# Kernel tuning notes

Hardware: AMD Instinct MI355X
Metric: run time of the kernel (lower is better)

## Reference

```python
import jax, jax.numpy as jnp
import numpy as np

B, T, V, U = 128, 256, 256, 2048


def setup_inputs() -> dict:
    key = jax.random.key(0)
    k_x, k_wx, k_wh, k_wd = jax.random.split(key, 4)
    x = jax.random.randint(k_x, (B, T), 0, V)
    # glorot-ish scaling so tanh doesn't saturate
    Wx = jax.random.normal(k_wx, (V, U), jnp.float32) * (1.0 / np.sqrt(V))
    Wh = jax.random.normal(k_wh, (U, U), jnp.float32) * (1.0 / np.sqrt(U))
    b = jnp.zeros((U,), jnp.float32)
    Wd = jax.random.normal(k_wd, (U, V), jnp.float32) * (1.0 / np.sqrt(U))
    bd = jnp.zeros((V,), jnp.float32)
    h0 = jnp.zeros((B, U), jnp.float32)
    return {"x": x, "Wx": Wx, "Wh": Wh, "b": b, "Wd": Wd, "bd": bd, "h0": h0}


def reference(x, Wx, Wh, b, Wd, bd, h0):
    # one_hot(x, V) @ Wx  ==  Wx[x]  (row gather; avoids materializing one-hot)
    x_proj = Wx[x] + b  # [B, T, U]
    x_proj_t = jnp.swapaxes(x_proj, 0, 1)  # [T, B, U] for scan

    def step(h, xt):
        # SimpleRNN cell: h_t = tanh(x_t Wx + h_{t-1} Wh + b)
        h_new = jnp.tanh(xt + h @ Wh)
        return h_new, h_new

    _, hs = jax.lax.scan(step, h0, x_proj_t)  # hs: [T, B, U]
    hs = jnp.swapaxes(hs, 0, 1)  # [B, T, U]
    logits = jnp.einsum('btu,uv->btv', hs, Wd) + bd  # [B, T, V]
    return logits
```

## Files before the change

### kernel.cpp

```cpp
#include <hip/hip_runtime.h>
#include <hip/hip_bf16.h>

#define B_ 128
#define T_ 256
#define V_ 256
#define U_ 2048

typedef __bf16 bf16x8 __attribute__((ext_vector_type(8)));
typedef float f32x4 __attribute__((ext_vector_type(4)));
typedef unsigned u32x4 __attribute__((ext_vector_type(4)));

union B8u { uint4 u; bf16x8 v; };

static __device__ inline bf16x8 u2b(uint4 u) { B8u t; t.u = u; return t.v; }
static __device__ inline bf16x8 ldg8(const unsigned short* p) {
    B8u t; t.u = *reinterpret_cast<const uint4*>(p); return t.v;
}
static __device__ inline bf16x8 lds8(const char* smem, unsigned off) {
    B8u t; t.u = *reinterpret_cast<const uint4*>(smem + off); return t.v;
}
static __device__ inline unsigned short f2b(float f) {
    __hip_bfloat16 h = __float2bfloat16(f);
    unsigned short r; __builtin_memcpy(&r, &h, 2); return r;
}
static __device__ inline uint4 ldg16_c(const unsigned short* p) {
    uint4 r;
    asm volatile("global_load_dwordx4 %0, %1, off"
                 : "=&v"(r) : "v"(p) : "memory");
    return r;
}
static __device__ inline void stg16_sc(unsigned short* p, u32x4 v) {
    asm volatile("global_store_dwordx4 %0, %1, off sc0 sc1"
                 :: "v"(p), "v"(v) : "memory");
}
static __device__ inline void stg4_sc_u32(unsigned* p, unsigned v) {
    asm volatile("global_store_dword %0, %1, off sc0 sc1"
                 :: "v"(p), "v"(v) : "memory");
}
static __device__ inline uint4 ldg16_sc_wait(const unsigned* p) {
    uint4 r;
    asm volatile("global_load_dwordx4 %0, %1, off sc0 sc1\n\ts_waitcnt vmcnt(0)"
                 : "=&v"(r) : "v"(p) : "memory");
    return r;
}
static __device__ inline float tanh_fast(float x) {
    float e = __expf(2.0f * x);
    return 1.0f - 2.0f * __builtin_amdgcn_rcpf(e + 1.0f);
}


__global__ void transpose_bf16(const float* __restrict__ in,
                               unsigned short* __restrict__ outp, int R, int C) {
    __shared__ float tile[32][33];
    int tc = blockIdx.x * 32, tr = blockIdx.y * 32;
    int lx = threadIdx.x & 31, ly = threadIdx.x >> 5;
#pragma unroll
    for (int i = 0; i < 32; i += 8)
        tile[ly + i][lx] = in[(size_t)(tr + ly + i) * C + tc + lx];
    __syncthreads();
#pragma unroll
    for (int i = 0; i < 32; i += 8)
        outp[(size_t)(tc + ly + i) * R + tr + lx] = f2b(tile[lx][ly + i]);
}

__global__ void prep_misc(const float* __restrict__ h0, unsigned short* __restrict__ hb,
                          const int* __restrict__ x, int* __restrict__ xT) {
    int i = blockIdx.x * 256 + threadIdx.x;
    hb[i] = f2b(h0[i]);
    if (i < B_ * T_) {
        int b = i >> 8, t = i & 255;
        xT[t * B_ + b] = x[i];
    }
}

__global__ __launch_bounds__(256, 1) void rnn_arc9(
        const int* __restrict__ xT, const float* __restrict__ Wx,
        const float* __restrict__ bias, const unsigned short* __restrict__ WhT,
        unsigned short* __restrict__ hs, unsigned* __restrict__ flags) {
    extern __shared__ char smem[];
    float* red = (float*)(smem + 32 * 2048 * 2);

    const int bid = blockIdx.x;
    const int g = bid >> 6, p = bid & 63;
    const int b0 = g * 32, c0 = p * 32;
    const int tid = threadIdx.x;
    const int w = tid >> 6, lane = tid & 63;
    const int lr = lane & 15, lh = lane >> 4;

    for (int i = tid; i < 32 * 256; i += 256) {
        int c = i >> 8, k8 = i & 255;
        uint4 v = *reinterpret_cast<const uint4*>(WhT + (size_t)(c0 + c) * U_ + k8 * 8);
        unsigned off = (unsigned)(c * 4096 + k8 * 16) ^ ((unsigned)(c & 7) << 4);
        *reinterpret_cast<uint4*>(smem + off) = v;
    }
    __syncthreads();

    const int kbase = w * 512;
    const unsigned lin0 = (unsigned)(lr * 4096) + (unsigned)((kbase + lh * 8) * 2);
    const unsigned lin1 = lin0 + 16 * 4096;
    const unsigned swz = (unsigned)(lr & 7) << 4;

    const bool epi = tid < 128;
    const int erow = tid >> 2;
    const int ec8 = (tid & 3) * 8;
    const int ucol = c0 + ec8;
    f32x4 bias4a = {0, 0, 0, 0}, bias4b = {0, 0, 0, 0};
    if (epi) {
        bias4a = *reinterpret_cast<const f32x4*>(bias + ucol);
        bias4b = *reinterpret_cast<const f32x4*>(bias + ucol + 4);
    }

    unsigned* myflag = flags + (unsigned)(g * 256 + p * 4 + w);
    const unsigned* pollp = flags + (unsigned)(g * 256 + lane * 4);

    f32x4 xpa = {0, 0, 0, 0}, xpb = {0, 0, 0, 0};
    if (epi) {
        int tok = xT[0 * B_ + b0 + erow];
        const float* wr = Wx + (size_t)tok * U_ + ucol;
        xpa = *reinterpret_cast<const f32x4*>(wr) + bias4a;
        xpb = *reinterpret_cast<const f32x4*>(wr + 4) + bias4b;
    }

    for (int t = 0; t < T_; ++t) {
        const unsigned short* hp = hs + (size_t)t * (B_ * U_);
        unsigned short* hc = hs + (size_t)(t + 1) * (B_ * U_);

        const unsigned short* pa0 = hp + (size_t)(b0 + lr) * U_ + kbase + lh * 8;
        const unsigned short* pa1 = pa0 + 16 * U_;
        uint4 areg0[16], areg1[16];
#pragma unroll
        for (int ks = 0; ks < 16; ++ks) {
            areg0[ks] = ldg16_c(pa0 + ks * 32);
            areg1[ks] = ldg16_c(pa1 + ks * 32);
        }
        asm volatile("s_waitcnt vmcnt(0)" ::: "memory");
        __builtin_amdgcn_sched_barrier(0);

        f32x4 acc00 = {0.f, 0.f, 0.f, 0.f}, acc01 = {0.f, 0.f, 0.f, 0.f};
        f32x4 acc10 = {0.f, 0.f, 0.f, 0.f}, acc11 = {0.f, 0.f, 0.f, 0.f};
#pragma unroll
        for (int ks = 0; ks < 16; ++ks) {
            bf16x8 a0 = u2b(areg0[ks]);
            bf16x8 a1 = u2b(areg1[ks]);
            bf16x8 bb0 = lds8(smem, (lin0 + (unsigned)ks * 64u) ^ swz);
            bf16x8 bb1 = lds8(smem, (lin1 + (unsigned)ks * 64u) ^ swz);
            acc00 = __builtin_amdgcn_mfma_f32_16x16x32_bf16(a0, bb0, acc00, 0, 0, 0);
            acc01 = __builtin_amdgcn_mfma_f32_16x16x32_bf16(a0, bb1, acc01, 0, 0, 0);
            acc10 = __builtin_amdgcn_mfma_f32_16x16x32_bf16(a1, bb0, acc10, 0, 0, 0);
            acc11 = __builtin_amdgcn_mfma_f32_16x16x32_bf16(a1, bb1, acc11, 0, 0, 0);
        }

        float* redw = red + w * 1152;
#pragma unroll
        for (int r = 0; r < 4; ++r) {
            redw[(lh * 4 + r) * 36 + lr] = acc00[r];
            redw[(lh * 4 + r) * 36 + 16 + lr] = acc01[r];
            redw[(16 + lh * 4 + r) * 36 + lr] = acc10[r];
            redw[(16 + lh * 4 + r) * 36 + 16 + lr] = acc11[r];
        }
        __syncthreads();

        if (epi) {
            const int o = erow * 36 + ec8;
            f32x4 za = *reinterpret_cast<f32x4*>(red + 0 * 1152 + o);
            f32x4 zb = *reinterpret_cast<f32x4*>(red + 0 * 1152 + o + 4);
            za += *reinterpret_cast<f32x4*>(red + 1 * 1152 + o);
            zb += *reinterpret_cast<f32x4*>(red + 1 * 1152 + o + 4);
            za += *reinterpret_cast<f32x4*>(red + 2 * 1152 + o);
            zb += *reinterpret_cast<f32x4*>(red + 2 * 1152 + o + 4);
            za += *reinterpret_cast<f32x4*>(red + 3 * 1152 + o);
            zb += *reinterpret_cast<f32x4*>(red + 3 * 1152 + o + 4);
            za += xpa;
            zb += xpb;
            u32x4 pk;
            pk.x = (unsigned)f2b(tanh_fast(za[0])) | ((unsigned)f2b(tanh_fast(za[1])) << 16);
            pk.y = (unsigned)f2b(tanh_fast(za[2])) | ((unsigned)f2b(tanh_fast(za[3])) << 16);
            pk.z = (unsigned)f2b(tanh_fast(zb[0])) | ((unsigned)f2b(tanh_fast(zb[1])) << 16);
            pk.w = (unsigned)f2b(tanh_fast(zb[2])) | ((unsigned)f2b(tanh_fast(zb[3])) << 16);
            stg16_sc(hc + (size_t)(b0 + erow) * U_ + ucol, pk);
        }

        asm volatile("s_waitcnt vmcnt(0)" ::: "memory");
        if (lane == 0) stg4_sc_u32(myflag, (unsigned)(t + 1));

        if (epi && t + 1 < T_) {
            int tok = xT[(t + 1) * B_ + b0 + erow];
            const float* wr = Wx + (size_t)tok * U_ + ucol;
            xpa = *reinterpret_cast<const f32x4*>(wr) + bias4a;
            xpb = *reinterpret_cast<const f32x4*>(wr + 4) + bias4b;
        }

        if (t + 1 < T_) {
            if (w == 0) {
                for (;;) {
                    uint4 f = ldg16_sc_wait(pollp);
                    unsigned m01 = f.x < f.y ? f.x : f.y;
                    unsigned m23 = f.z < f.w ? f.z : f.w;
                    unsigned m = m01 < m23 ? m01 : m23;
                    if (__all(m > (unsigned)t)) break;
                    __builtin_amdgcn_s_sleep(1);
                }
            }
            __syncthreads();
        }
    }
}

__global__ __launch_bounds__(256, 2) void decode_gemm2(
        const unsigned short* __restrict__ hsD, const unsigned short* __restrict__ WdT,
        const float* __restrict__ bdv, float* __restrict__ out) {
    const int tid = threadIdx.x;
    const int w = tid >> 6, lane = tid & 63;
    const int lr = lane & 15, lh = lane >> 4;
    const int r0 = blockIdx.x * 32;
    const int v0 = w * 64;

    const unsigned short* pa0 = hsD + (size_t)(r0 + lr) * U_ + lh * 8;
    const unsigned short* pa1 = pa0 + (size_t)16 * U_;
    const unsigned short* pb0 = WdT + (size_t)(v0 + lr) * U_ + lh * 8;

    f32x4 acc0[4], acc1[4];
#pragma unroll
    for (int n = 0; n < 4; ++n) {
        acc0[n] = (f32x4){0.f, 0.f, 0.f, 0.f};
        acc1[n] = (f32x4){0.f, 0.f, 0.f, 0.f};
    }

#pragma unroll 4
    for (int ks = 0; ks < 64; ++ks) {
        bf16x8 a0 = ldg8(pa0 + ks * 32);
        bf16x8 a1 = ldg8(pa1 + ks * 32);
#pragma unroll
        for (int n = 0; n < 4; ++n) {
            bf16x8 bb = ldg8(pb0 + (size_t)n * 16 * U_ + ks * 32);
            acc0[n] = __builtin_amdgcn_mfma_f32_16x16x32_bf16(a0, bb, acc0[n], 0, 0, 0);
            acc1[n] = __builtin_amdgcn_mfma_f32_16x16x32_bf16(a1, bb, acc1[n], 0, 0, 0);
        }
    }

#pragma unroll
    for (int n = 0; n < 4; ++n) {
        float bd_ = bdv[v0 + n * 16 + lr];
#pragma unroll
        for (int r = 0; r < 4; ++r) {
            int m0 = r0 + lh * 4 + r;
            int m1 = m0 + 16;
            out[((size_t)(m0 & 127) * T_ + (m0 >> 7)) * V_ + v0 + n * 16 + lr] =
                acc0[n][r] + bd_;
            out[((size_t)(m1 & 127) * T_ + (m1 >> 7)) * V_ + v0 + n * 16 + lr] =
                acc1[n][r] + bd_;
        }
    }
}

extern "C" void kernel_launch(void* const* d_in, const int* in_sizes, int n_in,
                              void* d_out, int out_size, void* d_ws, size_t ws_size,
                              hipStream_t stream) {
    const int* x = (const int*)d_in[0];
    const float* Wx = (const float*)d_in[1];
    const float* Wh = (const float*)d_in[2];
    const float* b = (const float*)d_in[3];
    const float* Wd = (const float*)d_in[4];
    const float* bd = (const float*)d_in[5];
    const float* h0 = (const float*)d_in[6];
    float* out = (float*)d_out;

    char* ws = (char*)d_ws;

    const size_t OFF_WhT = 0;
    const size_t OFF_WdT = 8388608;
    const size_t OFF_xT = 9437184;
    const size_t OFF_FLG = 9568256;
    const size_t OFF_HS = 9572352;

    unsigned short* WhT = (unsigned short*)(ws + OFF_WhT);
    unsigned short* WdT = (unsigned short*)(ws + OFF_WdT);
    int* xT = (int*)(ws + OFF_xT);
    unsigned* flags = (unsigned*)(ws + OFF_FLG);
    unsigned short* hs = (unsigned short*)(ws + OFF_HS);

    hipMemsetAsync(flags, 0, 4096, stream);
    transpose_bf16<<<dim3(64, 64), 256, 0, stream>>>(Wh, WhT, 2048, 2048);
    transpose_bf16<<<dim3(8, 64), 256, 0, stream>>>(Wd, WdT, 2048, 256);
    prep_misc<<<1024, 256, 0, stream>>>(h0, hs, x, xT);

    const int smem_bytes = 32 * 2048 * 2 + 4 * 1152 * 4;
    hipFuncSetAttribute((const void*)rnn_arc9, hipFuncAttributeMaxDynamicSharedMemorySize,
                        smem_bytes);
    void* args[] = {(void*)&xT, (void*)&Wx, (void*)&b, (void*)&WhT, (void*)&hs,
                    (void*)&flags};
    hipLaunchCooperativeKernel((const void*)rnn_arc9, dim3(256), dim3(256), args,
                               (unsigned)smem_bytes, stream);

    const unsigned short* hsD = hs + (size_t)B_ * U_;
    decode_gemm2<<<1024, 256, 0, stream>>>(hsD, WdT, bd, out);
}
```

Measured before the change: 1.800 ms.

## Fuse output projection into persistent RNN kernel using idle blocks per step

The decoder GEMM (hs @ Wd + bd) moves into the cooperative recurrent kernel. At each step, the first 16 column blocks of each batch group reuse the h_{t} tiles already loaded in registers to compute logits for step t-1 against a register-resident slice of WdT, with a one-step-delayed LDS reduction and store. This removes the separate decode kernel and its re-read of the full hidden-state history, but adds MFMA work, register pressure and LDS to every block's serial critical path. A fallback to the old two-kernel path is kept for when occupancy is insufficient.

```diff
diff --git a/kernel.cpp b/kernel.cpp
--- a/kernel.cpp
+++ b/kernel.cpp
@@ -73,12 +73,15 @@
     }
 }
 
-__global__ __launch_bounds__(256, 1) void rnn_arc9(
+__global__ __launch_bounds__(256, 1) void rnn_arc10(
         const int* __restrict__ xT, const float* __restrict__ Wx,
         const float* __restrict__ bias, const unsigned short* __restrict__ WhT,
-        unsigned short* __restrict__ hs, unsigned* __restrict__ flags) {
+        const unsigned short* __restrict__ WdT, const float* __restrict__ bdv,
+        unsigned short* __restrict__ hs, unsigned* __restrict__ flags,
+        float* __restrict__ out) {
     extern __shared__ char smem[];
-    float* red = (float*)(smem + 32 * 2048 * 2);
+    float* red = (float*)(smem + 131072);
+    float* dred = (float*)(smem + 149504);
 
     const int bid = blockIdx.x;
     const int g = bid >> 6, p = bid & 63;
@@ -99,6 +102,13 @@
     const unsigned lin0 = (unsigned)(lr * 4096) + (unsigned)((kbase + lh * 8) * 2);
     const unsigned lin1 = lin0 + 16 * 4096;
     const unsigned swz = (unsigned)(lr & 7) << 4;
+
+    const int v0 = (p & 15) * 16;
+    uint4 wdtreg[16];
+#pragma unroll
+    for (int ks = 0; ks < 16; ++ks)
+        wdtreg[ks] = *reinterpret_cast<const uint4*>(
+            WdT + (size_t)(v0 + lr) * U_ + kbase + lh * 8 + ks * 32);
 
     const bool epi = tid < 128;
     const int erow = tid >> 2;
@@ -109,6 +119,10 @@
         bias4a = *reinterpret_cast<const f32x4*>(bias + ucol);
         bias4b = *reinterpret_cast<const f32x4*>(bias + ucol + 4);
     }
+    const bool dstore = (p < 16) && epi;
+    const int dc4 = (tid & 3) * 4;
+    f32x4 bd4 = {0, 0, 0, 0};
+    if (dstore) bd4 = *reinterpret_cast<const f32x4*>(bdv + v0 + dc4);
 
     unsigned* myflag = flags + (unsigned)(g * 256 + p * 4 + w);
     const unsigned* pollp = flags + (unsigned)(g * 256 + lane * 4);
@@ -133,6 +147,18 @@
             areg0[ks] = ldg16_c(pa0 + ks * 32);
             areg1[ks] = ldg16_c(pa1 + ks * 32);
         }
+
+        if (dstore && t >= 2) {
+            const int o = erow * 20 + dc4;
+            f32x4 dz = *reinterpret_cast<f32x4*>(dred + 0 * 640 + o);
+            dz += *reinterpret_cast<f32x4*>(dred + 1 * 640 + o);
+            dz += *reinterpret_cast<f32x4*>(dred + 2 * 640 + o);
+            dz += *reinterpret_cast<f32x4*>(dred + 3 * 640 + o);
+            dz += bd4;
+            *reinterpret_cast<f32x4*>(
+                out + ((size_t)(b0 + erow) * T_ + (t - 2)) * V_ + v0 + dc4) = dz;
+        }
+
         asm volatile("s_waitcnt vmcnt(0)" ::: "memory");
         __builtin_amdgcn_sched_barrier(0);
 
@@ -183,6 +209,22 @@
         asm volatile("s_waitcnt vmcnt(0)" ::: "memory");
         if (lane == 0) stg4_sc_u32(myflag, (unsigned)(t + 1));
 
+        {
+            f32x4 dacc0 = {0.f, 0.f, 0.f, 0.f}, dacc1 = {0.f, 0.f, 0.f, 0.f};
+#pragma unroll
+            for (int ks = 0; ks < 16; ++ks) {
+                bf16x8 bw = u2b(wdtreg[ks]);
+                dacc0 = __builtin_amdgcn_mfma_f32_16x16x32_bf16(u2b(areg0[ks]), bw, dacc0, 0, 0, 0);
+                dacc1 = __builtin_amdgcn_mfma_f32_16x16x32_bf16(u2b(areg1[ks]), bw, dacc1, 0, 0, 0);
+            }
+            float* dredw = dred + w * 640;
+#pragma unroll
+            for (int r = 0; r < 4; ++r) {
+                dredw[(lh * 4 + r) * 20 + lr] = dacc0[r];
+                dredw[(16 + lh * 4 + r) * 20 + lr] = dacc1[r];
+            }
+        }
+
         if (epi && t + 1 < T_) {
             int tok = xT[(t + 1) * B_ + b0 + erow];
             const float* wr = Wx + (size_t)tok * U_ + ucol;
@@ -204,6 +246,200 @@
             __syncthreads();
         }
     }
+
+    __syncthreads();
+    if (dstore) {
+        const int o = erow * 20 + dc4;
+        f32x4 dz = *reinterpret_cast<f32x4*>(dred + 0 * 640 + o);
+        dz += *reinterpret_cast<f32x4*>(dred + 1 * 640 + o);
+        dz += *reinterpret_cast<f32x4*>(dred + 2 * 640 + o);
+        dz += *reinterpret_cast<f32x4*>(dred + 3 * 640 + o);
+        dz += bd4;
+        *reinterpret_cast<f32x4*>(
+            out + ((size_t)(b0 + erow) * T_ + (T_ - 2)) * V_ + v0 + dc4) = dz;
+    }
+
+    if (w == 0) {
+        for (;;) {
+            uint4 f = ldg16_sc_wait(pollp);
+            unsigned m01 = f.x < f.y ? f.x : f.y;
+            unsigned m23 = f.z < f.w ? f.z : f.w;
+            unsigned m = m01 < m23 ? m01 : m23;
+            if (__all(m > (unsigned)(T_ - 1))) break;
+            __builtin_amdgcn_s_sleep(1);
+        }
+    }
+    __syncthreads();
+
+    {
+        const unsigned short* paf =
+            hs + (size_t)T_ * (B_ * U_) + (size_t)(b0 + lr) * U_ + kbase + lh * 8;
+        uint4 fa0[16], fa1[16];
+#pragma unroll
+        for (int ks = 0; ks < 16; ++ks) {
+            fa0[ks] = ldg16_c(paf + ks * 32);
+            fa1[ks] = ldg16_c(paf + 16 * U_ + ks * 32);
+        }
+        asm volatile("s_waitcnt vmcnt(0)" ::: "memory");
+        __builtin_amdgcn_sched_barrier(0);
+        f32x4 dacc0 = {0.f, 0.f, 0.f, 0.f}, dacc1 = {0.f, 0.f, 0.f, 0.f};
+#pragma unroll
+        for (int ks = 0; ks < 16; ++ks) {
+            bf16x8 bw = u2b(wdtreg[ks]);
+            dacc0 = __builtin_amdgcn_mfma_f32_16x16x32_bf16(u2b(fa0[ks]), bw, dacc0, 0, 0, 0);
+            dacc1 = __builtin_amdgcn_mfma_f32_16x16x32_bf16(u2b(fa1[ks]), bw, dacc1, 0, 0, 0);
+        }
+        float* dredw = dred + w * 640;
+#pragma unroll
+        for (int r = 0; r < 4; ++r) {
+            dredw[(lh * 4 + r) * 20 + lr] = dacc0[r];
+            dredw[(16 + lh * 4 + r) * 20 + lr] = dacc1[r];
+        }
+    }
+    __syncthreads();
+    if (dstore) {
+        const int o = erow * 20 + dc4;
+        f32x4 dz = *reinterpret_cast<f32x4*>(dred + 0 * 640 + o);
+        dz += *reinterpret_cast<f32x4*>(dred + 1 * 640 + o);
+        dz += *reinterpret_cast<f32x4*>(dred + 2 * 640 + o);
+        dz += *reinterpret_cast<f32x4*>(dred + 3 * 640 + o);
+        dz += bd4;
+        *reinterpret_cast<f32x4*>(
+            out + ((size_t)(b0 + erow) * T_ + (T_ - 1)) * V_ + v0 + dc4) = dz;
+    }
+}
+
+__global__ __launch_bounds__(256, 1) void rnn_arc9(
+        const int* __restrict__ xT, const float* __restrict__ Wx,
+        const float* __restrict__ bias, const unsigned short* __restrict__ WhT,
+        unsigned short* __restrict__ hs, unsigned* __restrict__ flags) {
+    extern __shared__ char smem[];
+    float* red = (float*)(smem + 32 * 2048 * 2);
+
+    const int bid = blockIdx.x;
+    const int g = bid >> 6, p = bid & 63;
+    const int b0 = g * 32, c0 = p * 32;
+    const int tid = threadIdx.x;
+    const int w = tid >> 6, lane = tid & 63;
+    const int lr = lane & 15, lh = lane >> 4;
+
+    for (int i = tid; i < 32 * 256; i += 256) {
+        int c = i >> 8, k8 = i & 255;
+        uint4 v = *reinterpret_cast<const uint4*>(WhT + (size_t)(c0 + c) * U_ + k8 * 8);
+        unsigned off = (unsigned)(c * 4096 + k8 * 16) ^ ((unsigned)(c & 7) << 4);
+        *reinterpret_cast<uint4*>(smem + off) = v;
+    }
+    __syncthreads();
+
+    const int kbase = w * 512;
+    const unsigned lin0 = (unsigned)(lr * 4096) + (unsigned)((kbase + lh * 8) * 2);
+    const unsigned lin1 = lin0 + 16 * 4096;
+    const unsigned swz = (unsigned)(lr & 7) << 4;
+
+    const bool epi = tid < 128;
+    const int erow = tid >> 2;
+    const int ec8 = (tid & 3) * 8;
+    const int ucol = c0 + ec8;
+    f32x4 bias4a = {0, 0, 0, 0}, bias4b = {0, 0, 0, 0};
+    if (epi) {
+        bias4a = *reinterpret_cast<const f32x4*>(bias + ucol);
+        bias4b = *reinterpret_cast<const f32x4*>(bias + ucol + 4);
+    }
+
+    unsigned* myflag = flags + (unsigned)(g * 256 + p * 4 + w);
+    const unsigned* pollp = flags + (unsigned)(g * 256 + lane * 4);
+
+    f32x4 xpa = {0, 0, 0, 0}, xpb = {0, 0, 0, 0};
+    if (epi) {
+        int tok = xT[0 * B_ + b0 + erow];
+        const float* wr = Wx + (size_t)tok * U_ + ucol;
+        xpa = *reinterpret_cast<const f32x4*>(wr) + bias4a;
+        xpb = *reinterpret_cast<const f32x4*>(wr + 4) + bias4b;
+    }
+
+    for (int t = 0; t < T_; ++t) {
+        const unsigned short* hp = hs + (size_t)t * (B_ * U_);
+        unsigned short* hc = hs + (size_t)(t + 1) * (B_ * U_);
+
+        const unsigned short* pa0 = hp + (size_t)(b0 + lr) * U_ + kbase + lh * 8;
+        const unsigned short* pa1 = pa0 + 16 * U_;
+        uint4 areg0[16], areg1[16];
+#pragma unroll
+        for (int ks = 0; ks < 16; ++ks) {
+            areg0[ks] = ldg16_c(pa0 + ks * 32);
+            areg1[ks] = ldg16_c(pa1 + ks * 32);
+        }
+        asm volatile("s_waitcnt vmcnt(0)" ::: "memory");
+        __builtin_amdgcn_sched_barrier(0);
+
+        f32x4 acc00 = {0.f, 0.f, 0.f, 0.f}, acc01 = {0.f, 0.f, 0.f, 0.f};
+        f32x4 acc10 = {0.f, 0.f, 0.f, 0.f}, acc11 = {0.f, 0.f, 0.f, 0.f};
+#pragma unroll
+        for (int ks = 0; ks < 16; ++ks) {
+            bf16x8 a0 = u2b(areg0[ks]);
+            bf16x8 a1 = u2b(areg1[ks]);
+            bf16x8 bb0 = lds8(smem, (lin0 + (unsigned)ks * 64u) ^ swz);
+            bf16x8 bb1 = lds8(smem, (lin1 + (unsigned)ks * 64u) ^ swz);
+            acc00 = __builtin_amdgcn_mfma_f32_16x16x32_bf16(a0, bb0, acc00, 0, 0, 0);
+            acc01 = __builtin_amdgcn_mfma_f32_16x16x32_bf16(a0, bb1, acc01, 0, 0, 0);
+            acc10 = __builtin_amdgcn_mfma_f32_16x16x32_bf16(a1, bb0, acc10, 0, 0, 0);
+            acc11 = __builtin_amdgcn_mfma_f32_16x16x32_bf16(a1, bb1, acc11, 0, 0, 0);
+        }
+
+        float* redw = red + w * 1152;
+#pragma unroll
+        for (int r = 0; r < 4; ++r) {
+            redw[(lh * 4 + r) * 36 + lr] = acc00[r];
+            redw[(lh * 4 + r) * 36 + 16 + lr] = acc01[r];
+            redw[(16 + lh * 4 + r) * 36 + lr] = acc10[r];
+            redw[(16 + lh * 4 + r) * 36 + 16 + lr] = acc11[r];
+        }
+        __syncthreads();
+
+        if (epi) {
+            const int o = erow * 36 + ec8;
+            f32x4 za = *reinterpret_cast<f32x4*>(red + 0 * 1152 + o);
+            f32x4 zb = *reinterpret_cast<f32x4*>(red + 0 * 1152 + o + 4);
+            za += *reinterpret_cast<f32x4*>(red + 1 * 1152 + o);
+            zb += *reinterpret_cast<f32x4*>(red + 1 * 1152 + o + 4);
+            za += *reinterpret_cast<f32x4*>(red + 2 * 1152 + o);
+            zb += *reinterpret_cast<f32x4*>(red + 2 * 1152 + o + 4);
+            za += *reinterpret_cast<f32x4*>(red + 3 * 1152 + o);
+            zb += *reinterpret_cast<f32x4*>(red + 3 * 1152 + o + 4);
+            za += xpa;
+            zb += xpb;
+            u32x4 pk;
+            pk.x = (unsigned)f2b(tanh_fast(za[0])) | ((unsigned)f2b(tanh_fast(za[1])) << 16);
+            pk.y = (unsigned)f2b(tanh_fast(za[2])) | ((unsigned)f2b(tanh_fast(za[3])) << 16);
+            pk.z = (unsigned)f2b(tanh_fast(zb[0])) | ((unsigned)f2b(tanh_fast(zb[1])) << 16);
+            pk.w = (unsigned)f2b(tanh_fast(zb[2])) | ((unsigned)f2b(tanh_fast(zb[3])) << 16);
+            stg16_sc(hc + (size_t)(b0 + erow) * U_ + ucol, pk);
+        }
+
+        asm volatile("s_waitcnt vmcnt(0)" ::: "memory");
+        if (lane == 0) stg4_sc_u32(myflag, (unsigned)(t + 1));
+
+        if (epi && t + 1 < T_) {
+            int tok = xT[(t + 1) * B_ + b0 + erow];
+            const float* wr = Wx + (size_t)tok * U_ + ucol;
+            xpa = *reinterpret_cast<const f32x4*>(wr) + bias4a;
+            xpb = *reinterpret_cast<const f32x4*>(wr + 4) + bias4b;
+        }
+
+        if (t + 1 < T_) {
+            if (w == 0) {
+                for (;;) {
+                    uint4 f = ldg16_sc_wait(pollp);
+                    unsigned m01 = f.x < f.y ? f.x : f.y;
+                    unsigned m23 = f.z < f.w ? f.z : f.w;
+                    unsigned m = m01 < m23 ? m01 : m23;
+                    if (__all(m > (unsigned)t)) break;
+                    __builtin_amdgcn_s_sleep(1);
+                }
+            }
+            __syncthreads();
+        }
+    }
 }
 
 __global__ __launch_bounds__(256, 2) void decode_gemm2(
@@ -284,14 +520,27 @@
     transpose_bf16<<<dim3(8, 64), 256, 0, stream>>>(Wd, WdT, 2048, 256);
     prep_misc<<<1024, 256, 0, stream>>>(h0, hs, x, xT);
 
-    const int smem_bytes = 32 * 2048 * 2 + 4 * 1152 * 4;
-    hipFuncSetAttribute((const void*)rnn_arc9, hipFuncAttributeMaxDynamicSharedMemorySize,
-                        smem_bytes);
-    void* args[] = {(void*)&xT, (void*)&Wx, (void*)&b, (void*)&WhT, (void*)&hs,
-                    (void*)&flags};
-    hipLaunchCooperativeKernel((const void*)rnn_arc9, dim3(256), dim3(256), args,
-                               (unsigned)smem_bytes, stream);
-
-    const unsigned short* hsD = hs + (size_t)B_ * U_;
-    decode_gemm2<<<1024, 256, 0, stream>>>(hsD, WdT, bd, out);
-}
+    const int smem_fused = 131072 + 18432 + 10240;
+    hipFuncSetAttribute((const void*)rnn_arc10, hipFuncAttributeMaxDynamicSharedMemorySize,
+                        smem_fused);
+    int nb = 0;
+    hipError_t qerr = hipOccupancyMaxActiveBlocksPerMultiprocessor(
+        &nb, reinterpret_cast<const void*>(rnn_arc10), 256, (size_t)smem_fused);
+
+    if (qerr == hipSuccess && nb >= 1) {
+        void* args[] = {(void*)&xT, (void*)&Wx, (void*)&b,  (void*)&WhT, (void*)&WdT,
+                        (void*)&bd, (void*)&hs, (void*)&flags, (void*)&out};
+        hipLaunchCooperativeKernel((const void*)rnn_arc10, dim3(256), dim3(256), args,
+                                   (unsigned)smem_fused, stream);
+    } else {
+        const int smem9 = 32 * 2048 * 2 + 4 * 1152 * 4;
+        hipFuncSetAttribute((const void*)rnn_arc9, hipFuncAttributeMaxDynamicSharedMemorySize,
+                            smem9);
+        void* args9[] = {(void*)&xT, (void*)&Wx, (void*)&b, (void*)&WhT, (void*)&hs,
+                         (void*)&flags};
+        hipLaunchCooperativeKernel((const void*)rnn_arc9, dim3(256), dim3(256), args9,
+                                   (unsigned)smem9, stream);
+        const unsigned short* hsD = hs + (size_t)B_ * U_;
+        decode_gemm2<<<1024, 256, 0, stream>>>(hsD, WdT, bd, out);
+    }
+}
```

After: 1.800 ms. No clear change (-0.0%).
